# Kernel tuning notes

Hardware: AMD Instinct MI355X
Metric: run time of the kernel (lower is better)

## Reference

```python
import jax, jax.numpy as jnp
import numpy as np

B, S, D, H = 2, 2048, 1024, 16
HD = D // H          # 64
ROT = HD // 2        # 32

def _rope(x, cos, sin):
    # x: [B,S,H,HD] -> pairs [B,S,H,ROT,2]; cos/sin: [S,ROT] -> [1,S,1,ROT]
    x2 = x.reshape(x.shape[:3] + (ROT, 2))
    x0, x1 = x2[..., 0], x2[..., 1]
    c = cos[None, :, None, :]
    s = sin[None, :, None, :]
    out = jnp.stack([x0 * c - x1 * s, x1 * c + x0 * s], axis=-1)
    return out.reshape(x.shape)

def setup_inputs() -> dict:
    key = jax.random.key(0)
    ks = jax.random.split(key, 5)
    hidden_states = jax.random.normal(ks[0], (B, S, D), dtype=jnp.float32)
    # proper rotary cos/sin table: [S, ROT, 2]
    inv_freq = 1.0 / (10000.0 ** (np.arange(0, ROT, dtype=np.float32) / ROT))
    t = np.arange(S, dtype=np.float32)
    ang = np.outer(t, inv_freq)  # [S, ROT]
    freqs = jnp.asarray(np.stack([np.cos(ang), np.sin(ang)], axis=-1), dtype=jnp.float32)
    sc = 1.0 / np.sqrt(D)
    wq = jax.random.normal(ks[1], (D, D), dtype=jnp.float32) * sc
    wk = jax.random.normal(ks[2], (D, D), dtype=jnp.float32) * sc
    wv = jax.random.normal(ks[3], (D, D), dtype=jnp.float32) * sc
    wo = jax.random.normal(ks[4], (D, D), dtype=jnp.float32) * sc
    return {"hidden_states": hidden_states, "freqs": freqs, "wq": wq, "wk": wk, "wv": wv, "wo": wo}

def reference(hidden_states, freqs, wq, wk, wv, wo):
    b, s, _ = hidden_states.shape
    scaling = HD ** -0.5
    q = (hidden_states @ wq.T).reshape(b, s, H, HD)
    k = (hidden_states @ wk.T).reshape(b, s, H, HD)
    v = (hidden_states @ wv.T).reshape(b, s, H, HD)
    cos, sin = freqs[:s, :, 0], freqs[:s, :, 1]
    q = _rope(q, cos, sin)
    k = _rope(k, cos, sin)
    # [B,H,S,S] scores, fp32 softmax
    scores = jnp.einsum('bqhd,bkhd->bhqk', q, k) * scaling
    attn = jax.nn.softmax(scores.astype(jnp.float32), axis=-1).astype(q.dtype)
    out = jnp.einsum('bhqk,bkhd->bqhd', attn, v).reshape(b, s, D)
    return out @ wo.T
```

## Files before the change

kernel.cpp:

```cpp
#include <hip/hip_runtime.h>
#include <hip/hip_bf16.h>

typedef __attribute__((ext_vector_type(8))) short bf16x8;
typedef __attribute__((ext_vector_type(4))) float f32x4;
typedef __attribute__((ext_vector_type(16))) float f32x16;
typedef __attribute__((ext_vector_type(2))) float f32x2;
typedef unsigned short u16;

#define Bc   2
#define Sc   2048
#define Dc   1024
#define Hc   16
#define HDc  64
#define ROTc 32
#define Mrows 4096

__device__ __forceinline__ u16 f2bf(float x) {
  union { float f; unsigned u; } v{x};
  unsigned r = v.u + 0x7fffu + ((v.u >> 16) & 1u);
  return (u16)(r >> 16);
}
__device__ __forceinline__ float bf2f(u16 x) {
  union { unsigned u; float f; } v{(unsigned)x << 16};
  return v.f;
}
__device__ __forceinline__ unsigned cvtpk(float a, float b) {
  unsigned r;
  asm("v_cvt_pk_bf16_f32 %0, %1, %2" : "=v"(r) : "v"(a), "v"(b));
  return r;
}
__device__ __forceinline__ f32x2 pmax2(f32x2 a, f32x2 b) {
  f32x2 r;
  r.x = fmaxf(a.x, b.x);
  r.y = fmaxf(a.y, b.y);
  return r;
}

__device__ __forceinline__ void gload_lds16(const void* g, void* l) {
  __builtin_amdgcn_global_load_lds(
      (const __attribute__((address_space(1))) void*)g,
      (__attribute__((address_space(3))) void*)l, 16, 0, 0);
}

__global__ void cvt_all(const float* __restrict__ h, const float* __restrict__ q,
                        const float* __restrict__ k, const float* __restrict__ v,
                        const float* __restrict__ o,
                        u16* __restrict__ hb, u16* __restrict__ qb, u16* __restrict__ kb,
                        u16* __restrict__ vb, u16* __restrict__ ob) {
  size_t i = ((size_t)blockIdx.x * 256 + threadIdx.x) * 4;
  const float* s;
  u16* d;
  size_t off;
  if (i < (size_t)Mrows * Dc) {
    s = h; d = hb; off = i;
  } else {
    size_t j = i - (size_t)Mrows * Dc;
    int w = (int)(j >> 20);
    off = j & ((1u << 20) - 1);
    s = (w == 0) ? q : (w == 1) ? k : (w == 2) ? v : o;
    d = (w == 0) ? qb : (w == 1) ? kb : (w == 2) ? vb : ob;
  }
  float4 val = *reinterpret_cast<const float4*>(s + off);
  u16 r0 = f2bf(val.x), r1 = f2bf(val.y), r2 = f2bf(val.z), r3 = f2bf(val.w);
  ushort4 outv = {r0, r1, r2, r3};
  *reinterpret_cast<ushort4*>(d + off) = outv;
}

__global__ void gemm_qkv(const u16* __restrict__ A, const u16* __restrict__ W0,
                         const u16* __restrict__ W1, const u16* __restrict__ W2,
                         const float* __restrict__ freqs,
                         u16* __restrict__ Qo, u16* __restrict__ Ko,
                         u16* __restrict__ Vo) {
  __shared__ u16 As[128 * 32];
  __shared__ u16 Bs[128 * 32];
  const int orig = blockIdx.x;
  const int idx = orig >> 3;
  const int bx = (orig & 7) * 4 + (idx & 3);
  const int by = idx >> 2;
  const int wsel = by >> 3;
  const int n0 = (by & 7) * 128;
  const int m0 = bx * 128;
  const u16* Bm = (wsel == 0) ? W0 : (wsel == 1) ? W1 : W2;
  const int t = threadIdx.x;
  const int w = t >> 6;
  const int lane = t & 63;
  const int wm = w >> 1, wn = w & 1;
  const int c = lane & 15, g = lane >> 4;
  const int srow = t >> 2;
  const int skoff = ((t & 3) ^ (srow & 3)) * 8;

  f32x4 acc[4][4] = {};

  const u16* ag = A + (size_t)(m0 + srow) * Dc + skoff;
  const u16* bg = Bm + (size_t)(n0 + srow) * Dc + skoff;
  u16* al = &As[(w * 16) * 32];
  u16* bl = &Bs[(w * 16) * 32];

  for (int k0 = 0; k0 < Dc; k0 += 32) {
    gload_lds16(ag + k0, al);
    gload_lds16(ag + k0 + (size_t)64 * Dc, al + 64 * 32);
    gload_lds16(bg + k0, bl);
    gload_lds16(bg + k0 + (size_t)64 * Dc, bl + 64 * 32);
    __syncthreads();
    bf16x8 a[4], b[4];
#pragma unroll
    for (int f = 0; f < 4; ++f) {
      a[f] = *(const bf16x8*)&As[(wm * 64 + f * 16 + c) * 32 + (g ^ (c & 3)) * 8];
      b[f] = *(const bf16x8*)&Bs[(wn * 64 + f * 16 + c) * 32 + (g ^ (c & 3)) * 8];
    }
#pragma unroll
    for (int fm = 0; fm < 4; ++fm)
#pragma unroll
      for (int fn = 0; fn < 4; ++fn)
        acc[fm][fn] =
            __builtin_amdgcn_mfma_f32_16x16x32_bf16(a[fm], b[fn], acc[fm][fn], 0, 0, 0);
    __syncthreads();
  }

  u16* dst = (wsel == 0) ? Qo : (wsel == 1) ? Ko : Vo;
  const float qsc = (wsel == 0) ? 0.125f * 1.44269504f : 1.0f;
  const int codd = c & 1;
#pragma unroll
  for (int fm = 0; fm < 4; ++fm)
#pragma unroll
    for (int fn = 0; fn < 4; ++fn)
#pragma unroll
      for (int r = 0; r < 4; ++r) {
        const int m = m0 + wm * 64 + fm * 16 + g * 4 + r;
        const int n = n0 + wn * 64 + fn * 16 + c;
        float v = acc[fm][fn][r];
        const int b = m >> 11, s = m & (Sc - 1);
        const int hh = n >> 6, d = n & 63;
        size_t idx2;
        if (wsel < 2) {
          const float other = __shfl_xor(v, 1);
          const float2 f = reinterpret_cast<const float2*>(freqs)[s * ROTc + (d >> 1)];
          v = codd ? (v * f.x + other * f.y) : (v * f.x - other * f.y);
          v *= qsc;
          idx2 = (((size_t)(b * Hc + hh) * Sc) + s) * HDc + d;
        } else {
          idx2 = ((size_t)(b * Hc + hh) * HDc + d) * Sc + s;
        }
        dst[idx2] = f2bf(v);
      }
}

__global__ void gemm_out(const u16* __restrict__ A, const u16* __restrict__ Bm,
                         float* __restrict__ C) {
  __shared__ u16 As[64 * 32];
  __shared__ u16 Bs[128 * 32];
  const int m0 = blockIdx.x * 64;
  const int n0 = blockIdx.y * 128;
  const int t = threadIdx.x;
  const int w = t >> 6;
  const int lane = t & 63;
  const int wm = w >> 1, wn = w & 1;
  const int c = lane & 15, g = lane >> 4;
  const int srow = t >> 2;
  const int skoff = ((t & 3) ^ (srow & 3)) * 8;

  f32x4 acc[2][4] = {};

  const u16* ag = A + (size_t)(m0 + srow) * Dc + skoff;
  const u16* bg = Bm + (size_t)(n0 + srow) * Dc + skoff;
  u16* al = &As[(w * 16) * 32];
  u16* bl = &Bs[(w * 16) * 32];

  for (int k0 = 0; k0 < Dc; k0 += 32) {
    gload_lds16(ag + k0, al);
    gload_lds16(bg + k0, bl);
    gload_lds16(bg + k0 + (size_t)64 * Dc, bl + 64 * 32);
    __syncthreads();
    bf16x8 a[2], b[4];
#pragma unroll
    for (int f = 0; f < 2; ++f)
      a[f] = *(const bf16x8*)&As[(wm * 32 + f * 16 + c) * 32 + (g ^ (c & 3)) * 8];
#pragma unroll
    for (int f = 0; f < 4; ++f)
      b[f] = *(const bf16x8*)&Bs[(wn * 64 + f * 16 + c) * 32 + (g ^ (c & 3)) * 8];
#pragma unroll
    for (int fm = 0; fm < 2; ++fm)
#pragma unroll
      for (int fn = 0; fn < 4; ++fn)
        acc[fm][fn] =
            __builtin_amdgcn_mfma_f32_16x16x32_bf16(a[fm], b[fn], acc[fm][fn], 0, 0, 0);
    __syncthreads();
  }

#pragma unroll
  for (int fm = 0; fm < 2; ++fm)
#pragma unroll
    for (int fn = 0; fn < 4; ++fn)
#pragma unroll
      for (int r = 0; r < 4; ++r) {
        const int m = m0 + wm * 32 + fm * 16 + g * 4 + r;
        const int n = n0 + wn * 64 + fn * 16 + c;
        C[(size_t)m * Dc + n] = acc[fm][fn][r];
      }
}

__global__ __launch_bounds__(512, 2) void flash_attn(
    const u16* __restrict__ Q, const u16* __restrict__ Kb,
    const u16* __restrict__ Vt, u16* __restrict__ Ob) {
  __shared__ u16 smem[32768];
  const int orig = blockIdx.x;
  const int wg = (orig & 7) * 64 + (orig >> 3);
  const int bh = wg >> 4;
  const int q0 = (wg & 15) * 128;
  const int t = threadIdx.x, w = t >> 6, lane = t & 63;
  const int grp = w >> 2, wl = w & 3;
  const int ts = t & 255;
  const int l31 = lane & 31, hi = lane >> 5;
  const int sr = ts >> 4;
  const int su = (ts & 15) ^ (sr & 15);
  const int skv = sr + ((su >> 3) << 5);
  const int sd8 = (su & 7) * 8;
  const int rsw = (l31 & 15);

  const u16* Qp = Q + (size_t)bh * Sc * HDc;
  const u16* Kp = Kb + (size_t)bh * Sc * HDc;
  const u16* Vp = Vt + (size_t)bh * HDc * Sc;
  u16* const Kg = smem + grp * 8192;
  u16* const Vg = smem + 16384 + grp * 8192;

  const int q = q0 + wl * 32 + l31;
  bf16x8 aq[4];
#pragma unroll
  for (int kd = 0; kd < 4; ++kd)
    aq[kd] = *(const bf16x8*)(Qp + (size_t)q * HDc + kd * 16 + hi * 8);

  float m_run = -1e30f, l_run = 0.f;
  f32x16 o0 = {}, o1 = {};

  auto STAGE = [&](int tile, int bb) {
    const int base = grp * 1024 + tile * 64;
    gload_lds16(Kp + (size_t)(base + skv) * HDc + sd8, Kg + bb * 4096 + wl * 512);
    gload_lds16(Kp + (size_t)(base + skv + 16) * HDc + sd8,
                Kg + bb * 4096 + 2048 + wl * 512);
    gload_lds16(Vp + (size_t)skv * Sc + base + sd8, Vg + bb * 4096 + wl * 512);
    gload_lds16(Vp + (size_t)(skv + 16) * Sc + base + sd8,
                Vg + bb * 4096 + 2048 + wl * 512);
  };

  STAGE(0, 0);
  __syncthreads();

  int buf = 0;
  for (int tt = 0; tt < 16; ++tt) {
    if (tt + 1 < 16) STAGE(tt + 1, buf ^ 1);
    const u16* kb2 = Kg + buf * 4096;
    const u16* vb2 = Vg + buf * 4096;
    f32x16 s0 = {}, s1 = {};
    __builtin_amdgcn_s_setprio(1);
#pragma unroll
    for (int kd = 0; kd < 4; ++kd) {
      const int u0 = kd * 2 + hi;
      bf16x8 a0 = *(const bf16x8*)&kb2[l31 * 128 + (u0 ^ rsw) * 8];
      bf16x8 a1 = *(const bf16x8*)&kb2[l31 * 128 + ((u0 + 8) ^ rsw) * 8];
      s0 = __builtin_amdgcn_mfma_f32_32x32x16_bf16(a0, aq[kd], s0, 0, 0, 0);
      s1 = __builtin_amdgcn_mfma_f32_32x32x16_bf16(a1, aq[kd], s1, 0, 0, 0);
    }
    __builtin_amdgcn_s_setprio(0);
    f32x2 t4[4];
#pragma unroll
    for (int i = 0; i < 4; ++i) {
      f32x2 e0; e0.x = s0[2 * i]; e0.y = s0[2 * i + 1];
      f32x2 e1; e1.x = s0[2 * i + 8]; e1.y = s0[2 * i + 9];
      f32x2 e2; e2.x = s1[2 * i]; e2.y = s1[2 * i + 1];
      f32x2 e3; e3.x = s1[2 * i + 8]; e3.y = s1[2 * i + 9];
      t4[i] = pmax2(pmax2(e0, e1), pmax2(e2, e3));
    }
    f32x2 tp = pmax2(pmax2(t4[0], t4[1]), pmax2(t4[2], t4[3]));
    float mt = fmaxf(tp.x, tp.y);
    mt = fmaxf(mt, __shfl_xor(mt, 32));
    const bool skip = __all(mt <= m_run + 8.0f);
    if (!skip) {
      const float mn2 = fmaxf(m_run, mt);
      const float scl = __builtin_amdgcn_exp2f(m_run - mn2);
      m_run = mn2;
      l_run *= scl;
      o0 *= scl;
      o1 *= scl;
    }
    const float mn = m_run;
#pragma unroll
    for (int r = 0; r < 16; ++r) {
      s0[r] = __builtin_amdgcn_exp2f(s0[r] - mn);
      s1[r] = __builtin_amdgcn_exp2f(s1[r] - mn);
    }
    f32x2 ac;
    ac.x = 0.f; ac.y = 0.f;
#pragma unroll
    for (int i = 0; i < 8; ++i) {
      f32x2 e0; e0.x = s0[2 * i]; e0.y = s0[2 * i + 1];
      f32x2 e1; e1.x = s1[2 * i]; e1.y = s1[2 * i + 1];
      ac += e0 + e1;
    }
    float rs = ac.x + ac.y;
    rs += __shfl_xor(rs, 32);
    l_run += rs;
    unsigned pk0[8], pk1[8];
#pragma unroll
    for (int B = 0; B < 4; ++B)
#pragma unroll
      for (int s2 = 0; s2 < 2; ++s2) {
        pk0[B * 2 + s2] = cvtpk(s0[4 * B + 2 * s2], s0[4 * B + 2 * s2 + 1]);
        pk1[B * 2 + s2] = cvtpk(s1[4 * B + 2 * s2], s1[4 * B + 2 * s2 + 1]);
      }
#pragma unroll
    for (int ks = 0; ks < 4; ++ks) {
      const unsigned* pk = (ks >> 1) ? pk1 : pk0;
      const int m2 = (ks & 1) * 4;
      const unsigned A0 = pk[m2 + 0], A1 = pk[m2 + 1];
      const unsigned B0 = pk[m2 + 2], B1 = pk[m2 + 3];
      const unsigned L0 = hi ? B0 : A0, L1 = hi ? B1 : A1;
      const unsigned R0 = hi ? A0 : B0, R1 = hi ? A1 : B1;
      const unsigned X0 = __shfl_xor(R0, 32), X1 = __shfl_xor(R1, 32);
      union { unsigned u[4]; bf16x8 v; } bp;
      bp.u[0] = hi ? X0 : L0;
      bp.u[1] = hi ? X1 : L1;
      bp.u[2] = hi ? L0 : X0;
      bp.u[3] = hi ? L1 : X1;
      const int uv = ks * 2 + hi;
      bf16x8 va0 = *(const bf16x8*)&vb2[l31 * 128 + (uv ^ rsw) * 8];
      bf16x8 va1 = *(const bf16x8*)&vb2[l31 * 128 + ((uv + 8) ^ rsw) * 8];
      __builtin_amdgcn_s_setprio(1);
      o0 = __builtin_amdgcn_mfma_f32_32x32x16_bf16(va0, bp.v, o0, 0, 0, 0);
      o1 = __builtin_amdgcn_mfma_f32_32x32x16_bf16(va1, bp.v, o1, 0, 0, 0);
      __builtin_amdgcn_s_setprio(0);
    }
    __syncthreads();
    buf ^= 1;
  }

  float* fl = reinterpret_cast<float*>(smem);
  const int slot = (wl * 64 + lane) * 35;
  if (grp == 1) {
#pragma unroll
    for (int j = 0; j < 16; ++j) fl[slot + j] = o0[j];
#pragma unroll
    for (int j = 0; j < 16; ++j) fl[slot + 16 + j] = o1[j];
    fl[slot + 32] = m_run;
    fl[slot + 33] = l_run;
  }
  __syncthreads();
  if (grp == 0) {
    const float mB = fl[slot + 32], lB = fl[slot + 33];
    const float mx = fmaxf(m_run, mB);
    const float sA = __builtin_amdgcn_exp2f(m_run - mx);
    const float sB = __builtin_amdgcn_exp2f(mB - mx);
    const float rd = 1.0f / (l_run * sA + lB * sB);
    const float cA = sA * rd, cB = sB * rd;
    const int b = bh >> 4, hh = bh & 15;
    u16* orow = Ob + ((size_t)b * Sc + q) * Dc + hh * HDc;
#pragma unroll
    for (int B2 = 0; B2 < 4; ++B2) {
      const float v0 = o0[4 * B2 + 0] * cA + fl[slot + 4 * B2 + 0] * cB;
      const float v1 = o0[4 * B2 + 1] * cA + fl[slot + 4 * B2 + 1] * cB;
      const float v2 = o0[4 * B2 + 2] * cA + fl[slot + 4 * B2 + 2] * cB;
      const float v3 = o0[4 * B2 + 3] * cA + fl[slot + 4 * B2 + 3] * cB;
      uint2 pv;
      pv.x = cvtpk(v0, v1);
      pv.y = cvtpk(v2, v3);
      *reinterpret_cast<uint2*>(orow + 8 * B2 + 4 * hi) = pv;
    }
#pragma unroll
    for (int B2 = 0; B2 < 4; ++B2) {
      const float v0 = o1[4 * B2 + 0] * cA + fl[slot + 16 + 4 * B2 + 0] * cB;
      const float v1 = o1[4 * B2 + 1] * cA + fl[slot + 16 + 4 * B2 + 1] * cB;
      const float v2 = o1[4 * B2 + 2] * cA + fl[slot + 16 + 4 * B2 + 2] * cB;
      const float v3 = o1[4 * B2 + 3] * cA + fl[slot + 16 + 4 * B2 + 3] * cB;
      uint2 pv;
      pv.x = cvtpk(v0, v1);
      pv.y = cvtpk(v2, v3);
      *reinterpret_cast<uint2*>(orow + 32 + 8 * B2 + 4 * hi) = pv;
    }
  }
}

extern "C" void kernel_launch(void* const* d_in, const int* in_sizes, int n_in,
                              void* d_out, int out_size, void* d_ws, size_t ws_size,
                              hipStream_t stream) {
  (void)in_sizes; (void)n_in; (void)out_size; (void)ws_size;
  const float* hidden = (const float*)d_in[0];
  const float* freqs = (const float*)d_in[1];
  const float* wq = (const float*)d_in[2];
  const float* wk = (const float*)d_in[3];
  const float* wv = (const float*)d_in[4];
  const float* wo = (const float*)d_in[5];
  float* out = (float*)d_out;

  char* ws = (char*)d_ws;
  const size_t MB8 = (size_t)Mrows * Dc * 2;
  const size_t WB = (size_t)Dc * Dc * 2;
  u16* hb = (u16*)ws;  ws += MB8;
  u16* wqb = (u16*)ws; ws += WB;
  u16* wkb = (u16*)ws; ws += WB;
  u16* wvb = (u16*)ws; ws += WB;
  u16* wob = (u16*)ws; ws += WB;
  u16* qb = (u16*)ws;  ws += MB8;
  u16* kb = (u16*)ws;  ws += MB8;
  u16* vtb = (u16*)ws; ws += MB8;
  u16* ab = (u16*)ws;  ws += MB8;

  cvt_all<<<8192, 256, 0, stream>>>(hidden, wq, wk, wv, wo, hb, wqb, wkb, wvb, wob);
  gemm_qkv<<<768, 256, 0, stream>>>(hb, wqb, wkb, wvb, freqs, qb, kb, vtb);
  flash_attn<<<512, 512, 0, stream>>>(qb, kb, vtb, ab);
  gemm_out<<<dim3(64, 8), 256, 0, stream>>>(ab, wob, out);
}
```

Baseline: 129.6 us.

## Double-buffer LDS tiles in QKV and output projection GEMMs

Both projection GEMMs now use two LDS buffers per operand. The next K-slice's global-to-LDS load is issued before the current slice's MFMAs, so load latency overlaps compute and one barrier per iteration is removed. MFMA sections are also wrapped in s_setprio to favour the compute waves. This doubles LDS use per block, which may reduce occupancy, and the gemm_out staging code carries dead leftover expressions. It also relies on gload_lds16 completing by the single barrier that follows.

Result: no change. 128.0 us (-1.2%).

```diff
diff --git a/kernel.cpp b/kernel.cpp
--- a/kernel.cpp
+++ b/kernel.cpp
@@ -71,8 +71,8 @@
                          const float* __restrict__ freqs,
                          u16* __restrict__ Qo, u16* __restrict__ Ko,
                          u16* __restrict__ Vo) {
-  __shared__ u16 As[128 * 32];
-  __shared__ u16 Bs[128 * 32];
+  __shared__ u16 As[2][128 * 32];
+  __shared__ u16 Bs[2][128 * 32];
   const int orig = blockIdx.x;
   const int idx = orig >> 3;
   const int bx = (orig & 7) * 4 + (idx & 3);
@@ -93,28 +93,37 @@
 
   const u16* ag = A + (size_t)(m0 + srow) * Dc + skoff;
   const u16* bg = Bm + (size_t)(n0 + srow) * Dc + skoff;
-  u16* al = &As[(w * 16) * 32];
-  u16* bl = &Bs[(w * 16) * 32];
-
+  const int ldst = (w * 16) * 32;
+
+  auto STAGE = [&](int k0, int bb) {
+    gload_lds16(ag + k0, &As[bb][ldst]);
+    gload_lds16(ag + k0 + (size_t)64 * Dc, &As[bb][64 * 32 + ldst]);
+    gload_lds16(bg + k0, &Bs[bb][ldst]);
+    gload_lds16(bg + k0 + (size_t)64 * Dc, &Bs[bb][64 * 32 + ldst]);
+  };
+
+  STAGE(0, 0);
+  __syncthreads();
+
+  int buf = 0;
   for (int k0 = 0; k0 < Dc; k0 += 32) {
-    gload_lds16(ag + k0, al);
-    gload_lds16(ag + k0 + (size_t)64 * Dc, al + 64 * 32);
-    gload_lds16(bg + k0, bl);
-    gload_lds16(bg + k0 + (size_t)64 * Dc, bl + 64 * 32);
-    __syncthreads();
+    if (k0 + 32 < Dc) STAGE(k0 + 32, buf ^ 1);
     bf16x8 a[4], b[4];
 #pragma unroll
     for (int f = 0; f < 4; ++f) {
-      a[f] = *(const bf16x8*)&As[(wm * 64 + f * 16 + c) * 32 + (g ^ (c & 3)) * 8];
-      b[f] = *(const bf16x8*)&Bs[(wn * 64 + f * 16 + c) * 32 + (g ^ (c & 3)) * 8];
-    }
+      a[f] = *(const bf16x8*)&As[buf][(wm * 64 + f * 16 + c) * 32 + (g ^ (c & 3)) * 8];
+      b[f] = *(const bf16x8*)&Bs[buf][(wn * 64 + f * 16 + c) * 32 + (g ^ (c & 3)) * 8];
+    }
+    __builtin_amdgcn_s_setprio(1);
 #pragma unroll
     for (int fm = 0; fm < 4; ++fm)
 #pragma unroll
       for (int fn = 0; fn < 4; ++fn)
         acc[fm][fn] =
             __builtin_amdgcn_mfma_f32_16x16x32_bf16(a[fm], b[fn], acc[fm][fn], 0, 0, 0);
+    __builtin_amdgcn_s_setprio(0);
     __syncthreads();
+    buf ^= 1;
   }
 
   u16* dst = (wsel == 0) ? Qo : (wsel == 1) ? Ko : Vo;
@@ -147,8 +156,8 @@
 
 __global__ void gemm_out(const u16* __restrict__ A, const u16* __restrict__ Bm,
                          float* __restrict__ C) {
-  __shared__ u16 As[64 * 32];
-  __shared__ u16 Bs[128 * 32];
+  __shared__ u16 As[2][64 * 32];
+  __shared__ u16 Bs[2][128 * 32];
   const int m0 = blockIdx.x * 64;
   const int n0 = blockIdx.y * 128;
   const int t = threadIdx.x;
@@ -161,30 +170,43 @@
 
   f32x4 acc[2][4] = {};
 
-  const u16* ag = A + (size_t)(m0 + srow) * Dc + skoff;
+  const u16* ag = A + (size_t)(m0 + (srow & 63)) * Dc + skoff;
   const u16* bg = Bm + (size_t)(n0 + srow) * Dc + skoff;
-  u16* al = &As[(w * 16) * 32];
-  u16* bl = &Bs[(w * 16) * 32];
-
+  const int ldstA = ((w & 1) * 16 + (w >> 1) * 0) * 32;
+  const int ldstB = (w * 16) * 32;
+
+  auto STAGE = [&](int k0, int bb) {
+    if (w < 2) {
+    }
+    gload_lds16(ag + k0, &As[bb][(w * 16) * 32 - ((srow >= 64) ? 0 : 0)]);
+    gload_lds16(bg + k0, &Bs[bb][ldstB]);
+    gload_lds16(bg + k0 + (size_t)64 * Dc, &Bs[bb][64 * 32 + ldstB]);
+  };
+
+  (void)ldstA;
+  STAGE(0, 0);
+  __syncthreads();
+
+  int buf = 0;
   for (int k0 = 0; k0 < Dc; k0 += 32) {
-    gload_lds16(ag + k0, al);
-    gload_lds16(bg + k0, bl);
-    gload_lds16(bg + k0 + (size_t)64 * Dc, bl + 64 * 32);
-    __syncthreads();
+    if (k0 + 32 < Dc) STAGE(k0 + 32, buf ^ 1);
     bf16x8 a[2], b[4];
 #pragma unroll
     for (int f = 0; f < 2; ++f)
-      a[f] = *(const bf16x8*)&As[(wm * 32 + f * 16 + c) * 32 + (g ^ (c & 3)) * 8];
+      a[f] = *(const bf16x8*)&As[buf][(wm * 32 + f * 16 + c) * 32 + (g ^ (c & 3)) * 8];
 #pragma unroll
     for (int f = 0; f < 4; ++f)
-      b[f] = *(const bf16x8*)&Bs[(wn * 64 + f * 16 + c) * 32 + (g ^ (c & 3)) * 8];
+      b[f] = *(const bf16x8*)&Bs[buf][(wn * 64 + f * 16 + c) * 32 + (g ^ (c & 3)) * 8];
+    __builtin_amdgcn_s_setprio(1);
 #pragma unroll
     for (int fm = 0; fm < 2; ++fm)
 #pragma unroll
       for (int fn = 0; fn < 4; ++fn)
         acc[fm][fn] =
             __builtin_amdgcn_mfma_f32_16x16x32_bf16(a[fm], b[fn], acc[fm][fn], 0, 0, 0);
+    __builtin_amdgcn_s_setprio(0);
     __syncthreads();
+    buf ^= 1;
   }
 
 #pragma unroll
```

## Drop K/V double buffering in flash attention to cut shared memory

Applied to the files above, without the earlier changes.

The flash attention kernel now stages each K/V tile into a single shared-memory buffer and synchronises before computing on it, instead of prefetching the next tile into a second buffer. This roughly halves LDS use per block, presumably so more blocks can be resident per CU. The cost is that global-to-LDS loads no longer overlap the MFMA work, and each iteration gains an extra barrier. The reduction slot stride also changes from 35 to 34 so the buffer fits the smaller allocation, which may add bank conflicts. The edits to gemm_out have no effect on behaviour.

Result: no change. 128.5 us (-0.8%).

```diff
diff --git a/kernel.cpp b/kernel.cpp
--- a/kernel.cpp
+++ b/kernel.cpp
@@ -161,9 +161,9 @@
 
   f32x4 acc[2][4] = {};
 
-  const u16* ag = A + (size_t)(m0 + srow) * Dc + skoff;
+  const u16* ag = A + (size_t)(m0 + (srow & 63)) * Dc + skoff;
   const u16* bg = Bm + (size_t)(n0 + srow) * Dc + skoff;
-  u16* al = &As[(w * 16) * 32];
+  u16* al = &As[((t >> 2) & 63) * 0 + (w * 16) * 32];
   u16* bl = &Bs[(w * 16) * 32];
 
   for (int k0 = 0; k0 < Dc; k0 += 32) {
@@ -202,7 +202,7 @@
 __global__ __launch_bounds__(512, 2) void flash_attn(
     const u16* __restrict__ Q, const u16* __restrict__ Kb,
     const u16* __restrict__ Vt, u16* __restrict__ Ob) {
-  __shared__ u16 smem[32768];
+  __shared__ u16 smem[18432];
   const int orig = blockIdx.x;
   const int wg = (orig & 7) * 64 + (orig >> 3);
   const int bh = wg >> 4;
@@ -220,8 +220,8 @@
   const u16* Qp = Q + (size_t)bh * Sc * HDc;
   const u16* Kp = Kb + (size_t)bh * Sc * HDc;
   const u16* Vp = Vt + (size_t)bh * HDc * Sc;
-  u16* const Kg = smem + grp * 8192;
-  u16* const Vg = smem + 16384 + grp * 8192;
+  u16* const Kg = smem + grp * 4096;
+  u16* const Vg = smem + 8192 + grp * 4096;
 
   const int q = q0 + wl * 32 + l31;
   bf16x8 aq[4];
@@ -232,31 +232,24 @@
   float m_run = -1e30f, l_run = 0.f;
   f32x16 o0 = {}, o1 = {};
 
-  auto STAGE = [&](int tile, int bb) {
+  auto STAGE = [&](int tile) {
     const int base = grp * 1024 + tile * 64;
-    gload_lds16(Kp + (size_t)(base + skv) * HDc + sd8, Kg + bb * 4096 + wl * 512);
-    gload_lds16(Kp + (size_t)(base + skv + 16) * HDc + sd8,
-                Kg + bb * 4096 + 2048 + wl * 512);
-    gload_lds16(Vp + (size_t)skv * Sc + base + sd8, Vg + bb * 4096 + wl * 512);
-    gload_lds16(Vp + (size_t)(skv + 16) * Sc + base + sd8,
-                Vg + bb * 4096 + 2048 + wl * 512);
+    gload_lds16(Kp + (size_t)(base + skv) * HDc + sd8, Kg + wl * 512);
+    gload_lds16(Kp + (size_t)(base + skv + 16) * HDc + sd8, Kg + 2048 + wl * 512);
+    gload_lds16(Vp + (size_t)skv * Sc + base + sd8, Vg + wl * 512);
+    gload_lds16(Vp + (size_t)(skv + 16) * Sc + base + sd8, Vg + 2048 + wl * 512);
   };
 
-  STAGE(0, 0);
-  __syncthreads();
-
-  int buf = 0;
   for (int tt = 0; tt < 16; ++tt) {
-    if (tt + 1 < 16) STAGE(tt + 1, buf ^ 1);
-    const u16* kb2 = Kg + buf * 4096;
-    const u16* vb2 = Vg + buf * 4096;
+    STAGE(tt);
+    __syncthreads();
     f32x16 s0 = {}, s1 = {};
     __builtin_amdgcn_s_setprio(1);
 #pragma unroll
     for (int kd = 0; kd < 4; ++kd) {
       const int u0 = kd * 2 + hi;
-      bf16x8 a0 = *(const bf16x8*)&kb2[l31 * 128 + (u0 ^ rsw) * 8];
-      bf16x8 a1 = *(const bf16x8*)&kb2[l31 * 128 + ((u0 + 8) ^ rsw) * 8];
+      bf16x8 a0 = *(const bf16x8*)&Kg[l31 * 128 + (u0 ^ rsw) * 8];
+      bf16x8 a1 = *(const bf16x8*)&Kg[l31 * 128 + ((u0 + 8) ^ rsw) * 8];
       s0 = __builtin_amdgcn_mfma_f32_32x32x16_bf16(a0, aq[kd], s0, 0, 0, 0);
       s1 = __builtin_amdgcn_mfma_f32_32x32x16_bf16(a1, aq[kd], s1, 0, 0, 0);
     }
@@ -322,19 +315,18 @@
       bp.u[2] = hi ? L0 : X0;
       bp.u[3] = hi ? L1 : X1;
       const int uv = ks * 2 + hi;
-      bf16x8 va0 = *(const bf16x8*)&vb2[l31 * 128 + (uv ^ rsw) * 8];
-      bf16x8 va1 = *(const bf16x8*)&vb2[l31 * 128 + ((uv + 8) ^ rsw) * 8];
+      bf16x8 va0 = *(const bf16x8*)&Vg[l31 * 128 + (uv ^ rsw) * 8];
+      bf16x8 va1 = *(const bf16x8*)&Vg[l31 * 128 + ((uv + 8) ^ rsw) * 8];
       __builtin_amdgcn_s_setprio(1);
       o0 = __builtin_amdgcn_mfma_f32_32x32x16_bf16(va0, bp.v, o0, 0, 0, 0);
       o1 = __builtin_amdgcn_mfma_f32_32x32x16_bf16(va1, bp.v, o1, 0, 0, 0);
       __builtin_amdgcn_s_setprio(0);
     }
     __syncthreads();
-    buf ^= 1;
   }
 
   float* fl = reinterpret_cast<float*>(smem);
-  const int slot = (wl * 64 + lane) * 35;
+  const int slot = (wl * 64 + lane) * 34;
   if (grp == 1) {
 #pragma unroll
     for (int j = 0; j < 16; ++j) fl[slot + j] = o0[j];
```
